# Performance work log

Measured on AMD Instinct MI355X. Metric: run time of the kernel, lower is better.

Reference implementation:

```python
import jax, jax.numpy as jnp
import numpy as np

D_EMB = 128
N_CLASSES = 10
ITEM_DIM = 64


def _mlp(x, w1, b1, w2, b2):
    # torch nn.GELU default is exact (erf) gelu
    return jax.nn.gelu(x @ w1 + b1, approximate=False) @ w2 + b2


def sparsemax(z, axis=-1):
    """Euclidean projection of logits onto the probability simplex (sparsemax)."""
    n = z.shape[axis]
    z_sorted = -jnp.sort(-z, axis=axis)                      # descending
    ks = jnp.arange(1, n + 1, dtype=z.dtype)
    csum = jnp.cumsum(z_sorted, axis=axis)
    support = (1.0 + ks * z_sorted) > csum                   # broadcast over last axis
    k_z = jnp.sum(support, axis=axis, keepdims=True)         # support size
    csum_k = jnp.take_along_axis(csum, k_z.astype(jnp.int32) - 1, axis=axis)
    tau = (csum_k - 1.0) / k_z.astype(z.dtype)
    return jnp.maximum(z - tau, 0.0)


def setup_inputs() -> dict:
    key = jax.random.key(0)
    ks = jax.random.split(key, 22)
    d = D_EMB

    def lin(k, fan_in, fan_out):
        lim = (1.0 / fan_in) ** 0.5
        kw, kb = jax.random.split(k)
        w = jax.random.uniform(kw, (fan_in, fan_out), jnp.float32, -lim, lim)
        b = jax.random.uniform(kb, (fan_out,), jnp.float32, -lim, lim)
        return w, b

    wx1, bx1 = lin(ks[0], ITEM_DIM, d)
    wx2, bx2 = lin(ks[1], d, d)
    wq1, bq1 = lin(ks[2], 1, d)
    wq2, bq2 = lin(ks[3], d, d)
    wqp, bqp = lin(ks[4], d, d)
    wkp, bkp = lin(ks[5], d, d)
    wvp, bvp = lin(ks[6], d, d)
    wp1, bp1 = lin(ks[7], d, d)
    wp2, bp2 = lin(ks[8], d, N_CLASSES)

    x_items = jax.random.normal(ks[9], (32, 16384, ITEM_DIM), jnp.float32)
    x_query = jax.random.normal(ks[10], (32, 1), jnp.float32)
    return {
        "x_items": x_items, "x_query": x_query,
        "wx1": wx1, "bx1": bx1, "wx2": wx2, "bx2": bx2,
        "wq1": wq1, "bq1": bq1, "wq2": wq2, "bq2": bq2,
        "wqp": wqp, "bqp": bqp, "wkp": wkp, "bkp": bkp,
        "wvp": wvp, "bvp": bvp, "wp1": wp1, "bp1": bp1,
        "wp2": wp2, "bp2": bp2,
    }


def reference(x_items, x_query, wx1, bx1, wx2, bx2, wq1, bq1, wq2, bq2,
              wqp, bqp, wkp, bkp, wvp, bvp, wp1, bp1, wp2, bp2):
    # x_items: [B, N, item_dim]; x_query: [B, 1] -> unsqueeze(-1) -> [B, 1, 1]
    h_items = _mlp(x_items, wx1, bx1, wx2, bx2)              # [B, N, d]
    h_query = _mlp(x_query[..., None], wq1, bq1, wq2, bq2)   # [B, 1, d]
    q = h_query @ wqp + bqp                                   # [B, 1, d]
    k = h_items @ wkp + bkp                                   # [B, N, d]
    v = h_items @ wvp + bvp                                   # [B, N, d]
    scale = k.shape[-1] ** -0.5
    scores = jnp.einsum('bqd,bnd->bqn', q, k) * scale         # [B, 1, N]
    attn = sparsemax(scores, axis=-1)                         # simplex mapping
    z = jnp.einsum('bqn,bnd->bqd', attn, v)[:, 0]             # squeeze(1) -> [B, d]
    return _mlp(z, wp1, bp1, wp2, bp2)                        # [B, n_classes]
```

## Files before the change

### kernel.cpp

```cpp
#include <hip/hip_runtime.h>
#include <hip/hip_bf16.h>
#include <cstdint>

#define BATCH 32
#define NITEMS 16384
#define DEMB 128
#define IDIM 64

typedef short short8 __attribute__((ext_vector_type(8)));
typedef float f32x4 __attribute__((ext_vector_type(4)));

__device__ inline unsigned short f2bf(float f) {
    union { float f; unsigned int u; } v; v.f = f;
    unsigned int u = v.u;
    unsigned int r = (u + 0x7FFFu + ((u >> 16) & 1u)) >> 16;
    return (unsigned short)r;
}
__device__ inline float bf2f(unsigned short h) {
    union { unsigned int u; float f; } v; v.u = ((unsigned int)h) << 16;
    return v.f;
}

__device__ inline float gelu_f(float x) {
    float y = fabsf(x) * 0.70710678118654752f;
    float t = __builtin_amdgcn_rcpf(fmaf(0.3275911f, y, 1.0f));
    float p = fmaf(0.5307027145f, t, -0.7265760135f);
    p = fmaf(p, t, 0.7107068705f);
    p = fmaf(p, t, -0.142248368f);
    p = fmaf(p, t, 0.127414796f);
    p = p * t;
    float e = __builtin_amdgcn_exp2f(x * x * -0.72134752044448171f);
    float q = p * e;
    float phi = (x > 0.f) ? (1.0f - q) : q;
    return x * phi;
}

__global__ __launch_bounds__(128) void k0_prep(
    const float* __restrict__ xq, const float* __restrict__ wq1, const float* __restrict__ bq1,
    const float* __restrict__ wq2, const float* __restrict__ bq2,
    const float* __restrict__ wqp, const float* __restrict__ bqp,
    const float* __restrict__ wkp,
    const float* __restrict__ wx1, const float* __restrict__ wx2,
    float* __restrict__ r_out, unsigned short* __restrict__ w1h, unsigned short* __restrict__ w1l,
    int* __restrict__ ctr) {
    __shared__ float buf1[128], buf2[128], buf3[128], buf4[128];
    int t = threadIdx.x;
    int blk = blockIdx.x;
    if (blk < BATCH) {
        int b = blk;
        float xqv = xq[b];
        buf1[t] = gelu_f(fmaf(xqv, wq1[t], bq1[t]));
        __syncthreads();
        float acc = bq2[t];
        for (int j = 0; j < 128; j++) acc = fmaf(buf1[j], wq2[j * 128 + t], acc);
        buf2[t] = acc;
        __syncthreads();
        acc = bqp[t];
        for (int j = 0; j < 128; j++) acc = fmaf(buf2[j], wqp[j * 128 + t], acc);
        buf3[t] = acc;
        __syncthreads();
        acc = 0.f;
        for (int i = 0; i < 128; i++) acc = fmaf(wkp[t * 128 + i], buf3[i], acc);
        buf4[t] = acc * 0.08838834764831845f;
        __syncthreads();
        acc = 0.f;
        for (int i = 0; i < 128; i++) acc = fmaf(wx2[t * 128 + i], buf4[i], acc);
        r_out[b * 128 + t] = acc;
    } else {
        if (t < BATCH) ctr[t] = 0;
        for (int idx = t; idx < 64 * 128; idx += 128) {
            int k = idx >> 7, n = idx & 127;
            float v = wx1[idx];
            unsigned short hi = f2bf(v);
            float lo = v - bf2f(hi);
            w1h[n * 64 + k] = hi;
            w1l[n * 64 + k] = f2bf(lo);
        }
    }
}

__global__ __launch_bounds__(256) void k1_items(
    const float* __restrict__ x, const unsigned short* __restrict__ w1h,
    const unsigned short* __restrict__ w1l, const float* __restrict__ bx1,
    const float* __restrict__ r_in, float* __restrict__ scores) {
    __shared__ alignas(16) unsigned short lxh[64 * 72];
    __shared__ alignas(16) unsigned short lxl[64 * 72];
    __shared__ float red[4][64];
    int tid = threadIdx.x;
    int wave = tid >> 6, lane = tid & 63;
    int quad = lane >> 4, l15 = lane & 15;
    int tile = blockIdx.x;
    long item0 = (long)tile * 64;
    int b = tile >> 8;

    short8 wh[2][2], wl[2][2];
    for (int s = 0; s < 2; s++)
        for (int mt = 0; mt < 2; mt++) {
            int off = (wave * 32 + mt * 16 + l15) * 64 + s * 32 + quad * 8;
            wh[s][mt] = *(const short8*)(w1h + off);
            wl[s][mt] = *(const short8*)(w1l + off);
        }
    float bias8[2][4], rv8[2][4];
    for (int mt = 0; mt < 2; mt++)
        for (int rr = 0; rr < 4; rr++) {
            int row = wave * 32 + mt * 16 + quad * 4 + rr;
            bias8[mt][rr] = bx1[row];
            rv8[mt][rr] = r_in[b * 128 + row];
        }

    const float* xg = x + item0 * 64;
    for (int p = 0; p < 4; p++) {
        int idx = tid + p * 256;
        int row = idx >> 4, c4 = (idx & 15) * 4;
        float4 v = *(const float4*)(xg + row * 64 + c4);
        unsigned int ux = __float_as_uint(v.x), uy = __float_as_uint(v.y);
        unsigned int uz = __float_as_uint(v.z), uw = __float_as_uint(v.w);
        unsigned int hi01 = __builtin_amdgcn_perm(uy, ux, 0x07060302u);
        unsigned int hi23 = __builtin_amdgcn_perm(uw, uz, 0x07060302u);
        float lx = v.x - __uint_as_float(ux & 0xFFFF0000u);
        float ly = v.y - __uint_as_float(uy & 0xFFFF0000u);
        float lz = v.z - __uint_as_float(uz & 0xFFFF0000u);
        float lw = v.w - __uint_as_float(uw & 0xFFFF0000u);
        unsigned int lo01 = __builtin_amdgcn_perm(__float_as_uint(ly), __float_as_uint(lx), 0x07060302u);
        unsigned int lo23 = __builtin_amdgcn_perm(__float_as_uint(lw), __float_as_uint(lz), 0x07060302u);
        *(uint2*)(lxh + row * 72 + c4) = make_uint2(hi01, hi23);
        *(uint2*)(lxl + row * 72 + c4) = make_uint2(lo01, lo23);
    }
    __syncthreads();

    f32x4 acc[2][4];
    for (int mt = 0; mt < 2; mt++)
        for (int nt = 0; nt < 4; nt++) {
            f32x4 bi = {bias8[mt][0], bias8[mt][1], bias8[mt][2], bias8[mt][3]};
            acc[mt][nt] = bi;
        }

    for (int s = 0; s < 2; s++) {
        int koff = s * 32 + quad * 8;
        short8 xh[4], xl[4];
        for (int nt = 0; nt < 4; nt++) {
            int rb = (nt * 16 + l15) * 72 + koff;
            xh[nt] = *(const short8*)(lxh + rb);
            xl[nt] = *(const short8*)(lxl + rb);
        }
        for (int mt = 0; mt < 2; mt++)
            for (int nt = 0; nt < 4; nt++) {
                acc[mt][nt] = __builtin_amdgcn_mfma_f32_16x16x32_bf16(wh[s][mt], xl[nt], acc[mt][nt], 0, 0, 0);
                acc[mt][nt] = __builtin_amdgcn_mfma_f32_16x16x32_bf16(wl[s][mt], xh[nt], acc[mt][nt], 0, 0, 0);
                acc[mt][nt] = __builtin_amdgcn_mfma_f32_16x16x32_bf16(wh[s][mt], xh[nt], acc[mt][nt], 0, 0, 0);
            }
    }

    float pr[4] = {0.f, 0.f, 0.f, 0.f};
    for (int mt = 0; mt < 2; mt++)
        for (int nt = 0; nt < 4; nt++)
            for (int rr = 0; rr < 4; rr++) {
                float g = gelu_f(acc[mt][nt][rr]);
                pr[nt] = fmaf(g, rv8[mt][rr], pr[nt]);
            }
    for (int nt = 0; nt < 4; nt++) {
        pr[nt] += __shfl_xor(pr[nt], 16);
        pr[nt] += __shfl_xor(pr[nt], 32);
    }
    if (quad == 0)
        for (int nt = 0; nt < 4; nt++)
            red[wave][nt * 16 + l15] = pr[nt];
    __syncthreads();
    if (tid < 64)
        scores[item0 + tid] = red[0][tid] + red[1][tid] + red[2][tid] + red[3][tid];
}

__global__ __launch_bounds__(1024) void k2_tau(const float* __restrict__ scores,
                                               float* __restrict__ tau_out,
                                               float* __restrict__ u,
                                               int* __restrict__ ctr,
                                               int* __restrict__ sidx,
                                               float* __restrict__ swgt) {
    __shared__ float la[2][16], lc[2][16];
    int b = blockIdx.x, t = threadIdx.x;
    int wid = t >> 6, lane = t & 63;
    const float* s = scores + (size_t)b * NITEMS;
    float z[16];
    for (int i = 0; i < 16; i++) z[i] = s[t + i * 1024];
    float tau = -1e30f;
    for (int it = 0; it < 21; it++) {
        int pb = it & 1;
        float ls = 0.f, ct = 0.f;
        for (int i = 0; i < 16; i++) {
            bool a = z[i] > tau;
            ls += a ? z[i] : 0.f;
            ct += a ? 1.f : 0.f;
        }
        for (int off = 32; off; off >>= 1) {
            ls += __shfl_xor(ls, off);
            ct += __shfl_xor(ct, off);
        }
        if (lane == 0) { la[pb][wid] = ls; lc[pb][wid] = ct; }
        __syncthreads();
        float tls = 0.f, tct = 0.f;
        for (int i = 0; i < 16; i++) { tls += la[pb][i]; tct += lc[pb][i]; }
        float ntau = (tls - 1.0f) / tct;
        if (ntau == tau) break;
        tau = ntau;
    }
    if (t == 0) tau_out[b] = tau;
    if (t < 128) u[b * 128 + t] = 0.f;

    size_t lbase = (size_t)b * NITEMS;
    for (int i = 0; i < 16; i++) {
        bool hit = z[i] > tau;
        unsigned long long m = __ballot(hit);
        if (m) {
            int base = 0;
            if (lane == 0) base = atomicAdd(&ctr[b], (int)__popcll(m));
            base = __shfl(base, 0);
            if (hit) {
                int off = __popcll(m & ((1ULL << lane) - 1ULL));
                sidx[lbase + base + off] = t + i * 1024;
                swgt[lbase + base + off] = z[i] - tau;
            }
        }
    }
}

__global__ __launch_bounds__(256) void k3_support(
    const int* __restrict__ ctr, const int* __restrict__ sidx,
    const float* __restrict__ swgt, const float* __restrict__ x,
    const float* __restrict__ wx1, const float* __restrict__ bx1,
    const float* __restrict__ wx2, const float* __restrict__ bx2,
    float* __restrict__ u) {
    __shared__ float red[4][128];
    int blk = blockIdx.x;
    int b = blk >> 5;
    int sub = blk & 31;
    int wave = threadIdx.x >> 6, lane = threadIdx.x & 63;
    int wslot = sub * 4 + wave;
    int cnt = ctr[b];
    int t0 = lane, t1 = lane + 64;
    float bb0 = bx1[t0], bb1 = bx1[t1];
    float cc0 = bx2[t0], cc1 = bx2[t1];
    float u0 = 0.f, u1 = 0.f;
    size_t lbase = (size_t)b * NITEMS;
    for (int pos = wslot; pos < cnt; pos += 128) {
        float wgt = swgt[lbase + pos];
        int item = sidx[lbase + pos];
        const float* xr = x + ((size_t)b * NITEMS + item) * 64;
        float xv = xr[lane];
        float p0 = bb0, p1 = bb1;
        for (int k = 0; k < 64; k++) {
            float xk = __shfl(xv, k);
            p0 = fmaf(xk, wx1[k * 128 + t0], p0);
            p1 = fmaf(xk, wx1[k * 128 + t1], p1);
        }
        float h0 = gelu_f(p0), h1 = gelu_f(p1);
        float a0 = cc0, a1 = cc1;
        for (int j = 0; j < 64; j++) {
            float hj = __shfl(h0, j);
            a0 = fmaf(hj, wx2[j * 128 + t0], a0);
            a1 = fmaf(hj, wx2[j * 128 + t1], a1);
        }
        for (int j = 0; j < 64; j++) {
            float hj = __shfl(h1, j);
            a0 = fmaf(hj, wx2[(j + 64) * 128 + t0], a0);
            a1 = fmaf(hj, wx2[(j + 64) * 128 + t1], a1);
        }
        u0 = fmaf(wgt, a0, u0);
        u1 = fmaf(wgt, a1, u1);
    }
    red[wave][t0] = u0;
    red[wave][t1] = u1;
    __syncthreads();
    if (threadIdx.x < 128) {
        float s = red[0][threadIdx.x] + red[1][threadIdx.x] +
                  red[2][threadIdx.x] + red[3][threadIdx.x];
        atomicAdd(&u[b * 128 + threadIdx.x], s);
    }
}

__global__ __launch_bounds__(128) void k4_head(
    const float* __restrict__ u, const float* __restrict__ wvp, const float* __restrict__ bvp,
    const float* __restrict__ wp1, const float* __restrict__ bp1,
    const float* __restrict__ wp2, const float* __restrict__ bp2,
    float* __restrict__ out) {
    __shared__ float ub[128], zb[128], tb[128];
    int b = blockIdx.x, t = threadIdx.x;
    ub[t] = u[b * 128 + t];
    __syncthreads();
    float z = bvp[t];
    for (int j = 0; j < 128; j++) z = fmaf(ub[j], wvp[j * 128 + t], z);
    zb[t] = z;
    __syncthreads();
    float h = bp1[t];
    for (int j = 0; j < 128; j++) h = fmaf(zb[j], wp1[j * 128 + t], h);
    tb[t] = gelu_f(h);
    __syncthreads();
    if (t < 10) {
        float o = bp2[t];
        for (int j = 0; j < 128; j++) o = fmaf(tb[j], wp2[j * 10 + t], o);
        out[b * 10 + t] = o;
    }
}

extern "C" void kernel_launch(void* const* d_in, const int* in_sizes, int n_in,
                              void* d_out, int out_size, void* d_ws, size_t ws_size,
                              hipStream_t stream) {
    const float* x_items = (const float*)d_in[0];
    const float* x_query = (const float*)d_in[1];
    const float* wx1 = (const float*)d_in[2];
    const float* bx1 = (const float*)d_in[3];
    const float* wx2 = (const float*)d_in[4];
    const float* bx2 = (const float*)d_in[5];
    const float* wq1 = (const float*)d_in[6];
    const float* bq1 = (const float*)d_in[7];
    const float* wq2 = (const float*)d_in[8];
    const float* bq2 = (const float*)d_in[9];
    const float* wqp = (const float*)d_in[10];
    const float* bqp = (const float*)d_in[11];
    const float* wkp = (const float*)d_in[12];
    const float* wvp = (const float*)d_in[14];
    const float* bvp = (const float*)d_in[15];
    const float* wp1 = (const float*)d_in[16];
    const float* bp1 = (const float*)d_in[17];
    const float* wp2 = (const float*)d_in[18];
    const float* bp2 = (const float*)d_in[19];
    float* out = (float*)d_out;

    char* ws = (char*)d_ws;
    float* r_buf        = (float*)(ws);
    unsigned short* w1h = (unsigned short*)(ws + 16384);
    unsigned short* w1l = (unsigned short*)(ws + 32768);
    float* scores       = (float*)(ws + 49152);
    float* tau          = (float*)(ws + 2146304);
    float* u            = (float*)(ws + 2146560);
    int*   ctr          = (int*)  (ws + 2162944);
    int*   sidx         = (int*)  (ws + 2163200);
    float* swgt         = (float*)(ws + 4260352);

    k0_prep<<<33, 128, 0, stream>>>(x_query, wq1, bq1, wq2, bq2, wqp, bqp, wkp,
                                    wx1, wx2, r_buf, w1h, w1l, ctr);
    k1_items<<<(BATCH * NITEMS) / 64, 256, 0, stream>>>(x_items, w1h, w1l, bx1, r_buf, scores);
    k2_tau<<<BATCH, 1024, 0, stream>>>(scores, tau, u, ctr, sidx, swgt);
    k3_support<<<BATCH * 32, 256, 0, stream>>>(ctr, sidx, swgt, x_items,
                                               wx1, bx1, wx2, bx2, u);
    k4_head<<<BATCH, 128, 0, stream>>>(u, wvp, bvp, wp1, bp1, wp2, bp2, out);
}
```

Baseline: 327.5 us.

## Defer second item-MLP layer past sparsemax sum and use MFMA for support rows

Because the sparsemax weights sum to one, the second item-MLP layer (wx2, bx2) is moved after the weighted sum and applied once per batch in the head kernel. The support kernel then only computes the first layer. It does this with split-bf16 MFMA on 64-row gathered tiles, replacing the per-item scalar FMA loops. The compaction in k2 now reserves one atomic slot range per wave instead of one per ballot. The bias-after-sum rewrite relies on the weights summing to one, and the gelu outputs keep fp32 accumulation via the hi/lo split.

```diff
diff --git a/kernel.cpp b/kernel.cpp
--- a/kernel.cpp
+++ b/kernel.cpp
@@ -172,7 +172,7 @@
 
 __global__ __launch_bounds__(1024) void k2_tau(const float* __restrict__ scores,
                                                float* __restrict__ tau_out,
-                                               float* __restrict__ u,
+                                               float* __restrict__ vbuf,
                                                int* __restrict__ ctr,
                                                int* __restrict__ sidx,
                                                float* __restrict__ swgt) {
@@ -204,87 +204,147 @@
         tau = ntau;
     }
     if (t == 0) tau_out[b] = tau;
-    if (t < 128) u[b * 128 + t] = 0.f;
+    if (t < 128) vbuf[b * 128 + t] = 0.f;
 
     size_t lbase = (size_t)b * NITEMS;
+    unsigned long long m[16];
+    int tot = 0;
     for (int i = 0; i < 16; i++) {
-        bool hit = z[i] > tau;
-        unsigned long long m = __ballot(hit);
-        if (m) {
-            int base = 0;
-            if (lane == 0) base = atomicAdd(&ctr[b], (int)__popcll(m));
-            base = __shfl(base, 0);
-            if (hit) {
-                int off = __popcll(m & ((1ULL << lane) - 1ULL));
-                sidx[lbase + base + off] = t + i * 1024;
-                swgt[lbase + base + off] = z[i] - tau;
-            }
-        }
+        m[i] = __ballot(z[i] > tau);
+        tot += (int)__popcll(m[i]);
+    }
+    int base = 0;
+    if (lane == 0 && tot) base = atomicAdd(&ctr[b], tot);
+    base = __shfl(base, 0);
+    unsigned long long lmask = (1ULL << lane) - 1ULL;
+    for (int i = 0; i < 16; i++) {
+        if (z[i] > tau) {
+            int off = (int)__popcll(m[i] & lmask);
+            sidx[lbase + base + off] = t + i * 1024;
+            swgt[lbase + base + off] = z[i] - tau;
+        }
+        base += (int)__popcll(m[i]);
     }
 }
 
 __global__ __launch_bounds__(256) void k3_support(
     const int* __restrict__ ctr, const int* __restrict__ sidx,
     const float* __restrict__ swgt, const float* __restrict__ x,
-    const float* __restrict__ wx1, const float* __restrict__ bx1,
-    const float* __restrict__ wx2, const float* __restrict__ bx2,
-    float* __restrict__ u) {
-    __shared__ float red[4][128];
+    const unsigned short* __restrict__ w1h, const unsigned short* __restrict__ w1l,
+    const float* __restrict__ bx1, float* __restrict__ vbuf) {
+    __shared__ alignas(16) unsigned short lxh[64 * 72];
+    __shared__ alignas(16) unsigned short lxl[64 * 72];
+    __shared__ int litem[64];
+    int tid = threadIdx.x;
+    int wave = tid >> 6, lane = tid & 63;
+    int quad = lane >> 4, l15 = lane & 15;
     int blk = blockIdx.x;
-    int b = blk >> 5;
-    int sub = blk & 31;
-    int wave = threadIdx.x >> 6, lane = threadIdx.x & 63;
-    int wslot = sub * 4 + wave;
+    int b = blk >> 3;
+    int sub = blk & 7;
     int cnt = ctr[b];
-    int t0 = lane, t1 = lane + 64;
-    float bb0 = bx1[t0], bb1 = bx1[t1];
-    float cc0 = bx2[t0], cc1 = bx2[t1];
-    float u0 = 0.f, u1 = 0.f;
     size_t lbase = (size_t)b * NITEMS;
-    for (int pos = wslot; pos < cnt; pos += 128) {
-        float wgt = swgt[lbase + pos];
-        int item = sidx[lbase + pos];
-        const float* xr = x + ((size_t)b * NITEMS + item) * 64;
-        float xv = xr[lane];
-        float p0 = bb0, p1 = bb1;
-        for (int k = 0; k < 64; k++) {
-            float xk = __shfl(xv, k);
-            p0 = fmaf(xk, wx1[k * 128 + t0], p0);
-            p1 = fmaf(xk, wx1[k * 128 + t1], p1);
-        }
-        float h0 = gelu_f(p0), h1 = gelu_f(p1);
-        float a0 = cc0, a1 = cc1;
-        for (int j = 0; j < 64; j++) {
-            float hj = __shfl(h0, j);
-            a0 = fmaf(hj, wx2[j * 128 + t0], a0);
-            a1 = fmaf(hj, wx2[j * 128 + t1], a1);
-        }
-        for (int j = 0; j < 64; j++) {
-            float hj = __shfl(h1, j);
-            a0 = fmaf(hj, wx2[(j + 64) * 128 + t0], a0);
-            a1 = fmaf(hj, wx2[(j + 64) * 128 + t1], a1);
-        }
-        u0 = fmaf(wgt, a0, u0);
-        u1 = fmaf(wgt, a1, u1);
-    }
-    red[wave][t0] = u0;
-    red[wave][t1] = u1;
-    __syncthreads();
-    if (threadIdx.x < 128) {
-        float s = red[0][threadIdx.x] + red[1][threadIdx.x] +
-                  red[2][threadIdx.x] + red[3][threadIdx.x];
-        atomicAdd(&u[b * 128 + threadIdx.x], s);
-    }
+
+    short8 wh[2][2], wl[2][2];
+    for (int s = 0; s < 2; s++)
+        for (int mt = 0; mt < 2; mt++) {
+            int off = (wave * 32 + mt * 16 + l15) * 64 + s * 32 + quad * 8;
+            wh[s][mt] = *(const short8*)(w1h + off);
+            wl[s][mt] = *(const short8*)(w1l + off);
+        }
+    float bias8[2][4];
+    for (int mt = 0; mt < 2; mt++)
+        for (int rr = 0; rr < 4; rr++)
+            bias8[mt][rr] = bx1[wave * 32 + mt * 16 + quad * 4 + rr];
+
+    float vacc[2][4] = {{0.f, 0.f, 0.f, 0.f}, {0.f, 0.f, 0.f, 0.f}};
+
+    int ntiles = (cnt + 63) >> 6;
+    for (int tt = sub; tt < ntiles; tt += 8) {
+        int tstart = tt * 64;
+        __syncthreads();
+        if (tid < 64) {
+            int pos = tstart + tid;
+            litem[tid] = (pos < cnt) ? sidx[lbase + pos] : 0;
+        }
+        __syncthreads();
+        for (int p = 0; p < 4; p++) {
+            int idx = tid + p * 256;
+            int row = idx >> 4, c4 = (idx & 15) * 4;
+            const float* xr = x + (lbase + (size_t)litem[row]) * 64;
+            float4 v = *(const float4*)(xr + c4);
+            unsigned int ux = __float_as_uint(v.x), uy = __float_as_uint(v.y);
+            unsigned int uz = __float_as_uint(v.z), uw = __float_as_uint(v.w);
+            unsigned int hi01 = __builtin_amdgcn_perm(uy, ux, 0x07060302u);
+            unsigned int hi23 = __builtin_amdgcn_perm(uw, uz, 0x07060302u);
+            float lx = v.x - __uint_as_float(ux & 0xFFFF0000u);
+            float ly = v.y - __uint_as_float(uy & 0xFFFF0000u);
+            float lz = v.z - __uint_as_float(uz & 0xFFFF0000u);
+            float lw = v.w - __uint_as_float(uw & 0xFFFF0000u);
+            unsigned int lo01 = __builtin_amdgcn_perm(__float_as_uint(ly), __float_as_uint(lx), 0x07060302u);
+            unsigned int lo23 = __builtin_amdgcn_perm(__float_as_uint(lw), __float_as_uint(lz), 0x07060302u);
+            *(uint2*)(lxh + row * 72 + c4) = make_uint2(hi01, hi23);
+            *(uint2*)(lxl + row * 72 + c4) = make_uint2(lo01, lo23);
+        }
+        __syncthreads();
+
+        float wv[4];
+        for (int nt = 0; nt < 4; nt++) {
+            int pos = tstart + nt * 16 + l15;
+            wv[nt] = (pos < cnt) ? swgt[lbase + pos] : 0.f;
+        }
+
+        f32x4 acc[2][4];
+        for (int mt = 0; mt < 2; mt++)
+            for (int nt = 0; nt < 4; nt++) {
+                f32x4 bi = {bias8[mt][0], bias8[mt][1], bias8[mt][2], bias8[mt][3]};
+                acc[mt][nt] = bi;
+            }
+        for (int s = 0; s < 2; s++) {
+            int koff = s * 32 + quad * 8;
+            short8 xh[4], xl[4];
+            for (int nt = 0; nt < 4; nt++) {
+                int rb = (nt * 16 + l15) * 72 + koff;
+                xh[nt] = *(const short8*)(lxh + rb);
+                xl[nt] = *(const short8*)(lxl + rb);
+            }
+            for (int mt = 0; mt < 2; mt++)
+                for (int nt = 0; nt < 4; nt++) {
+                    acc[mt][nt] = __builtin_amdgcn_mfma_f32_16x16x32_bf16(wh[s][mt], xl[nt], acc[mt][nt], 0, 0, 0);
+                    acc[mt][nt] = __builtin_amdgcn_mfma_f32_16x16x32_bf16(wl[s][mt], xh[nt], acc[mt][nt], 0, 0, 0);
+                    acc[mt][nt] = __builtin_amdgcn_mfma_f32_16x16x32_bf16(wh[s][mt], xh[nt], acc[mt][nt], 0, 0, 0);
+                }
+        }
+        for (int mt = 0; mt < 2; mt++)
+            for (int nt = 0; nt < 4; nt++)
+                for (int rr = 0; rr < 4; rr++)
+                    vacc[mt][rr] = fmaf(wv[nt], gelu_f(acc[mt][nt][rr]), vacc[mt][rr]);
+    }
+
+    for (int mt = 0; mt < 2; mt++)
+        for (int rr = 0; rr < 4; rr++) {
+            float vs = vacc[mt][rr];
+            vs += __shfl_xor(vs, 1);
+            vs += __shfl_xor(vs, 2);
+            vs += __shfl_xor(vs, 4);
+            vs += __shfl_xor(vs, 8);
+            if (l15 == 0)
+                atomicAdd(&vbuf[b * 128 + wave * 32 + mt * 16 + quad * 4 + rr], vs);
+        }
 }
 
 __global__ __launch_bounds__(128) void k4_head(
-    const float* __restrict__ u, const float* __restrict__ wvp, const float* __restrict__ bvp,
+    const float* __restrict__ v, const float* __restrict__ wx2, const float* __restrict__ bx2,
+    const float* __restrict__ wvp, const float* __restrict__ bvp,
     const float* __restrict__ wp1, const float* __restrict__ bp1,
     const float* __restrict__ wp2, const float* __restrict__ bp2,
     float* __restrict__ out) {
-    __shared__ float ub[128], zb[128], tb[128];
+    __shared__ float vb[128], ub[128], zb[128], tb[128];
     int b = blockIdx.x, t = threadIdx.x;
-    ub[t] = u[b * 128 + t];
+    vb[t] = v[b * 128 + t];
+    __syncthreads();
+    float uacc = bx2[t];
+    for (int j = 0; j < 128; j++) uacc = fmaf(vb[j], wx2[j * 128 + t], uacc);
+    ub[t] = uacc;
     __syncthreads();
     float z = bvp[t];
     for (int j = 0; j < 128; j++) z = fmaf(ub[j], wvp[j * 128 + t], z);
@@ -331,7 +391,7 @@
     unsigned short* w1l = (unsigned short*)(ws + 32768);
     float* scores       = (float*)(ws + 49152);
     float* tau          = (float*)(ws + 2146304);
-    float* u            = (float*)(ws + 2146560);
+    float* vbuf         = (float*)(ws + 2146560);
     int*   ctr          = (int*)  (ws + 2162944);
     int*   sidx         = (int*)  (ws + 2163200);
     float* swgt         = (float*)(ws + 4260352);
@@ -339,8 +399,8 @@
     k0_prep<<<33, 128, 0, stream>>>(x_query, wq1, bq1, wq2, bq2, wqp, bqp, wkp,
                                     wx1, wx2, r_buf, w1h, w1l, ctr);
     k1_items<<<(BATCH * NITEMS) / 64, 256, 0, stream>>>(x_items, w1h, w1l, bx1, r_buf, scores);
-    k2_tau<<<BATCH, 1024, 0, stream>>>(scores, tau, u, ctr, sidx, swgt);
-    k3_support<<<BATCH * 32, 256, 0, stream>>>(ctr, sidx, swgt, x_items,
-                                               wx1, bx1, wx2, bx2, u);
-    k4_head<<<BATCH, 128, 0, stream>>>(u, wvp, bvp, wp1, bp1, wp2, bp2, out);
-}
+    k2_tau<<<BATCH, 1024, 0, stream>>>(scores, tau, vbuf, ctr, sidx, swgt);
+    k3_support<<<BATCH * 8, 256, 0, stream>>>(ctr, sidx, swgt, x_items,
+                                              w1h, w1l, bx1, vbuf);
+    k4_head<<<BATCH, 128, 0, stream>>>(vbuf, wx2, bx2, wvp, bvp, wp1, bp1, wp2, bp2, out);
+}
```

Result: faster. 292.5 us (-10.7%).
